# Performance work log

Hardware: AMD Instinct MI355X
Metric: run time of the kernel (lower is better)

## Reference

```python
import jax, jax.numpy as jnp
import numpy as np

D_IN = 1024
D_OUT = 1024
NUM_HEADS = 16
HEAD_DIM = D_OUT // NUM_HEADS


def setup_inputs() -> dict:
    key = jax.random.key(0)
    k1, k2, k3, k4 = jax.random.split(key, 4)
    x = jax.random.normal(k1, (2, 2048, D_IN), dtype=jnp.float32)
    # Linear weights stored torch-style [out_features, in_features]
    W_qkv = jax.random.normal(k2, (3 * D_OUT, D_IN), dtype=jnp.float32) * (1.0 / np.sqrt(D_IN))
    W_out = jax.random.normal(k3, (D_OUT, D_OUT), dtype=jnp.float32) * (1.0 / np.sqrt(D_OUT))
    b_out = jax.random.normal(k4, (D_OUT,), dtype=jnp.float32) * 0.01
    return {"x": x, "W_qkv": W_qkv, "W_out": W_out, "b_out": b_out}


def reference(x, W_qkv, W_out, b_out):
    b, s, _ = x.shape
    qkv = jnp.einsum('bsi,oi->bso', x, W_qkv)  # [b, s, 3*d_out]
    q, k, v = jnp.split(qkv, 3, axis=-1)
    def to_heads(t):
        return t.reshape(b, s, NUM_HEADS, HEAD_DIM).transpose(0, 2, 1, 3)
    q, k, v = to_heads(q), to_heads(k), to_heads(v)
    # NOTE: original module does NOT scale by 1/sqrt(head_dim)
    scores = jnp.einsum('bhqd,bhkd->bhqk', q, k)
    causal = jnp.tril(jnp.ones((s, s), dtype=bool))  # True = keep
    scores = jnp.where(causal[None, None], scores, -jnp.inf)
    attn = jax.nn.softmax(scores, axis=-1)
    ctx = jnp.einsum('bhqk,bhkd->bhqd', attn, v)
    ctx = ctx.transpose(0, 2, 1, 3).reshape(b, s, D_OUT)
    return jnp.einsum('bso,po->bsp', ctx, W_out) + b_out
```

## Files before the change

### kernel.cpp

```cpp
#include <hip/hip_runtime.h>
#include <cstdint>
#include <cstddef>


typedef __attribute__((ext_vector_type(8))) short bf16x8;
typedef __attribute__((ext_vector_type(4))) short bf16x4;
typedef __attribute__((ext_vector_type(4))) float f32x4;

#define LOG2E 1.44269504f

#define MFMA16(a, b, c) __builtin_amdgcn_mfma_f32_16x16x32_bf16((a), (b), (c), 0, 0, 0)

#if defined(__HIP_DEVICE_COMPILE__)
  #if __has_builtin(__builtin_amdgcn_mfma_f32_16x16x16bf16_1k)
    #define MFMAK16(a, b, c) __builtin_amdgcn_mfma_f32_16x16x16bf16_1k((a), (b), (c), 0, 0, 0)
  #elif __has_builtin(__builtin_amdgcn_mfma_f32_16x16x16_bf16)
    #define MFMAK16(a, b, c) __builtin_amdgcn_mfma_f32_16x16x16_bf16((a), (b), (c), 0, 0, 0)
  #else
    #error "no 16x16x16 bf16 MFMA builtin on device"
  #endif
#else
  #define MFMAK16(a, b, c) (c)
#endif

#define GLDS16(g, s)                                                        \
  __builtin_amdgcn_global_load_lds(                                         \
      (const __attribute__((address_space(1))) void*)(g),                   \
      (__attribute__((address_space(3))) void*)(s), 16, 0, 0)

#define ASYNC_BAR(N) asm volatile("s_waitcnt vmcnt(" #N ")\n\ts_barrier" ::: "memory")
#define BAR() asm volatile("s_barrier" ::: "memory")

static __device__ __forceinline__ float exp2_hw(float x) {
  float r;
  asm("v_exp_f32 %0, %1" : "=v"(r) : "v"(x));
  return r;
}
#define EXP2F(x) exp2_hw(x)

static __device__ __forceinline__ unsigned short f2bf(float f) {
  unsigned int u = __builtin_bit_cast(unsigned int, f);
  u += 0x7FFFu + ((u >> 16) & 1u);
  return (unsigned short)(u >> 16);
}

static __device__ __forceinline__ unsigned int pk2bf(float a, float b) {
  const unsigned int ua = __builtin_bit_cast(unsigned int, a) + 0x8000u;
  const unsigned int ub = __builtin_bit_cast(unsigned int, b) + 0x8000u;
  return __builtin_amdgcn_perm(ub, ua, 0x07060302);
}

__global__ __launch_bounds__(256) void cast_bf16(const float* __restrict__ x,
                                                 const float* __restrict__ wq,
                                                 const float* __restrict__ wo,
                                                 unsigned short* __restrict__ xb,
                                                 unsigned short* __restrict__ wqb,
                                                 unsigned short* __restrict__ wob)
{
  const int id = blockIdx.x * 256 + threadIdx.x;
  const float* src;
  unsigned short* dst;
  int off;
  if (id < 1048576)               { src = x;  dst = xb;  off = id; }
  else if (id < 1048576 + 786432) { src = wq; dst = wqb; off = id - 1048576; }
  else                            { src = wo; dst = wob; off = id - (1048576 + 786432); }
  float4 v = ((const float4*)src)[off];
  ushort4 o;
  o.x = f2bf(v.x); o.y = f2bf(v.y); o.z = f2bf(v.z); o.w = f2bf(v.w);
  ((ushort4*)dst)[off] = o;
}

#define MMAC(AF, BF, MS, NS)                                                       \
  do {                                                                             \
    __builtin_amdgcn_s_setprio(1);                                                 \
    if (swapped) {                                                                 \
      _Pragma("unroll")                                                            \
      for (int mt = 0; mt < 4; ++mt)                                               \
        _Pragma("unroll")                                                          \
        for (int nt = 0; nt < 2; ++nt) {                                           \
          acc[(MS)*4+mt][(NS)*2+nt] = MFMA16(BF[nt][0], AF[mt][0], acc[(MS)*4+mt][(NS)*2+nt]); \
          acc[(MS)*4+mt][(NS)*2+nt] = MFMA16(BF[nt][1], AF[mt][1], acc[(MS)*4+mt][(NS)*2+nt]); \
        }                                                                          \
    } else {                                                                       \
      _Pragma("unroll")                                                            \
      for (int mt = 0; mt < 4; ++mt)                                               \
        _Pragma("unroll")                                                          \
        for (int nt = 0; nt < 2; ++nt) {                                           \
          acc[(MS)*4+mt][(NS)*2+nt] = MFMA16(AF[mt][0], BF[nt][0], acc[(MS)*4+mt][(NS)*2+nt]); \
          acc[(MS)*4+mt][(NS)*2+nt] = MFMA16(AF[mt][1], BF[nt][1], acc[(MS)*4+mt][(NS)*2+nt]); \
        }                                                                          \
    }                                                                              \
    __builtin_amdgcn_s_setprio(0);                                                 \
  } while (0)

__global__ __launch_bounds__(512, 2) void gemm_qkv(const unsigned short* __restrict__ A,
                                                   const unsigned short* __restrict__ B,
                                                   unsigned short* __restrict__ Qb,
                                                   unsigned short* __restrict__ Kb,
                                                   unsigned short* __restrict__ Vt)
{
  __shared__ unsigned short pool[65536];

  const int tid  = threadIdx.x;
  const int wave = tid >> 6, lane = tid & 63, quad = lane >> 4, cl = lane & 15;
  const int wm = wave >> 2, wn = wave & 3;

  const int bid = blockIdx.x;
  const int xcd = bid & 7, j = bid >> 3;
  const int mb = (xcd >> 1) * 4 + j / 6;
  const int nb = (xcd & 1) * 6 + j % 6;
  const int m0 = mb * 256, n0 = nb * 256;
  const int part = nb >> 2;
  const bool swapped = (part < 2);

  const int lrow = lane >> 3;
  const int sg   = (lane & 7) ^ lrow;

  auto stageA = [&](int h0, int buf, int k0) {
    #pragma unroll
    for (int ii = 0; ii < 2; ++ii) {
      const int r0 = h0 + wave * 16 + ii * 8;
      GLDS16(A + (size_t)(m0 + r0 + lrow) * 1024 + k0 + sg * 8,
             &pool[buf * 32768 + r0 * 64]);
    }
  };
  auto stageB = [&](int h0, int buf, int k0) {
    #pragma unroll
    for (int ii = 0; ii < 2; ++ii) {
      const int r0 = h0 + wave * 16 + ii * 8;
      GLDS16(B + (size_t)(n0 + r0 + lrow) * 1024 + k0 + sg * 8,
             &pool[buf * 32768 + 16384 + r0 * 64]);
    }
  };

  const int rswz = cl & 7;
  auto loadA = [&](bf16x8 (&af)[4][2], int msub, int b) {
    const unsigned short* base = &pool[b * 32768];
    #pragma unroll
    for (int mt = 0; mt < 4; ++mt) {
      const int row = wm * 128 + msub * 64 + mt * 16 + cl;
      #pragma unroll
      for (int kk = 0; kk < 2; ++kk)
        af[mt][kk] = *(const bf16x8*)&base[row * 64 + ((kk * 4 + quad) ^ rswz) * 8];
    }
  };
  auto loadB = [&](bf16x8 (&bf)[2][2], int nsub, int b) {
    const unsigned short* base = &pool[b * 32768 + 16384];
    #pragma unroll
    for (int nt = 0; nt < 2; ++nt) {
      const int row = wn * 64 + nsub * 32 + nt * 16 + cl;
      #pragma unroll
      for (int kk = 0; kk < 2; ++kk)
        bf[nt][kk] = *(const bf16x8*)&base[row * 64 + ((kk * 4 + quad) ^ rswz) * 8];
    }
  };

  f32x4 acc[8][4];
  #pragma unroll
  for (int i = 0; i < 8; ++i)
    #pragma unroll
    for (int jj = 0; jj < 4; ++jj)
      #pragma unroll
      for (int r = 0; r < 4; ++r) acc[i][jj][r] = 0.f;

  stageB(0,   0, 0);
  stageA(0,   0, 0);
  stageB(128, 0, 0);
  stageA(128, 0, 0);
  stageB(0,   1, 64);
  stageA(0,   1, 64);

  #pragma unroll 1
  for (int t = 0; t < 16; ++t) {
    const int b = t & 1, bn = b ^ 1;
    const int kc  = (t + 1) * 64;
    const int kc2 = (t + 2) * 64;

    bf16x8 af[4][2], bfA[2][2], bfB[2][2];

    if (t < 15) { ASYNC_BAR(4); } else { ASYNC_BAR(0); }
    loadA(af, 0, b);
    loadB(bfA, 0, b);
    if (t < 15) stageB(128, bn, kc);
    MMAC(af, bfA, 0, 0);

    loadB(bfB, 1, b);
    if (t < 15) stageA(128, bn, kc);
    MMAC(af, bfB, 0, 1);

    BAR();
    loadA(af, 1, b);
    if (t < 14) stageB(0, b, kc2);
    MMAC(af, bfB, 1, 1);

    BAR();
    if (t < 14) stageA(0, b, kc2);
    MMAC(af, bfA, 1, 0);
  }

  const int bb = m0 >> 11, ss = m0 & 2047;
  if (part < 2) {
    unsigned short* dst = (part == 0) ? Qb : Kb;
    const float sc2 = (part == 0) ? LOG2E : 1.0f;
    const int npb = (n0 & 1023) + wn * 64;
    #pragma unroll
    for (int mt = 0; mt < 8; ++mt) {
      const int m = ss + wm * 128 + mt * 16 + cl;
      #pragma unroll
      for (int nt = 0; nt < 4; ++nt) {
        const int np = npb + nt * 16 + quad * 4;
        const int hh = np >> 6, d0 = np & 63;
        ushort4 pk;
        pk.x = f2bf(acc[mt][nt][0] * sc2);
        pk.y = f2bf(acc[mt][nt][1] * sc2);
        pk.z = f2bf(acc[mt][nt][2] * sc2);
        pk.w = f2bf(acc[mt][nt][3] * sc2);
        *(ushort4*)&dst[((size_t)(bb * 16 + hh) * 2048 + m) * 64 + d0] = pk;
      }
    }
  } else {
    unsigned short* trans = pool;
    #pragma unroll 1
    for (int r = 0; r < 2; ++r) {
      __syncthreads();
      if ((wn >> 1) == r) {
        #pragma unroll
        for (int mt = 0; mt < 8; ++mt) {
          const int s_l = wm * 128 + mt * 16 + quad * 4;
          #pragma unroll
          for (int nt = 0; nt < 4; ++nt) {
            const int n_l = (wn & 1) * 64 + nt * 16 + cl;
            ushort4 pk;
            pk.x = f2bf(acc[mt][nt][0]); pk.y = f2bf(acc[mt][nt][1]);
            pk.z = f2bf(acc[mt][nt][2]); pk.w = f2bf(acc[mt][nt][3]);
            *(ushort4*)&trans[n_l * 264 + s_l] = pk;
          }
        }
      }
      __syncthreads();
      const int row = tid >> 2, q4 = tid & 3;
      const int nv = (n0 & 1023) + r * 128 + row;
      const int hh = nv >> 6, d = nv & 63;
      unsigned short* drow = Vt + ((size_t)(bb * 16 + hh) * 64 + d) * 2048 + ss + q4 * 64;
      #pragma unroll
      for (int i = 0; i < 8; ++i)
        *(bf16x8*)(drow + i * 8) = *(const bf16x8*)&trans[row * 264 + q4 * 64 + i * 8];
    }
  }
}

__global__ __launch_bounds__(256) void gemm_obt(const unsigned short* __restrict__ A,
                                                const unsigned short* __restrict__ B,
                                                const float* __restrict__ bias,
                                                float* __restrict__ OutF)
{
  __shared__ unsigned short pool[24576];

  const int tid  = threadIdx.x;
  const int wave = tid >> 6, lane = tid & 63, quad = lane >> 4, cl = lane & 15;
  const int wm = wave >> 1, wn = wave & 1;
  const int m0 = blockIdx.y * 128, n0 = blockIdx.x * 128;
  const int sr = lane >> 2, sc = lane & 3;

  f32x4 acc[4][4];
  #pragma unroll
  for (int i = 0; i < 4; ++i)
    #pragma unroll
    for (int j = 0; j < 4; ++j)
      #pragma unroll
      for (int r = 0; r < 4; ++r) acc[i][j][r] = 0.f;

  const int scs = (sc ^ ((sr >> 1) & 3)) * 8;
  const int rchunk = (quad ^ ((cl >> 1) & 3)) * 8;

  auto stage = [&](int k0, int buf) {
    unsigned short* As = pool + buf * 8192;
    unsigned short* Bs = As + 4096;
    #pragma unroll
    for (int ii = 0; ii < 2; ++ii) {
      const int r = wave * 32 + ii * 16 + sr;
      GLDS16(A + (size_t)(m0 + r) * 1024 + k0 + scs, &As[(wave * 32 + ii * 16) * 32]);
      GLDS16(B + (size_t)(n0 + r) * 1024 + k0 + scs, &Bs[(wave * 32 + ii * 16) * 32]);
    }
  };

  stage(0, 0);
  stage(32, 1);
  int cur = 0;
  #pragma unroll 1
  for (int it = 0; it < 32; ++it) {
    if (it + 2 < 32) {
      ASYNC_BAR(4);
      const int bnx = (cur == 0) ? 2 : cur - 1;
      stage((it + 2) * 32, bnx);
    } else if (it + 1 < 32) {
      ASYNC_BAR(4);
    } else {
      ASYNC_BAR(0);
    }

    const unsigned short* As = pool + cur * 8192;
    const unsigned short* Bs = As + 4096;
    bf16x8 af[4], bfr[4];
    #pragma unroll
    for (int mt = 0; mt < 4; ++mt)
      af[mt] = *(const bf16x8*)&As[(wm * 64 + mt * 16 + cl) * 32 + rchunk];
    #pragma unroll
    for (int nt = 0; nt < 4; ++nt)
      bfr[nt] = *(const bf16x8*)&Bs[(wn * 64 + nt * 16 + cl) * 32 + rchunk];

    __builtin_amdgcn_s_setprio(1);
    #pragma unroll
    for (int mt = 0; mt < 4; ++mt)
      #pragma unroll
      for (int nt = 0; nt < 4; ++nt)
        acc[mt][nt] = MFMA16(bfr[nt], af[mt], acc[mt][nt]);
    __builtin_amdgcn_s_setprio(0);
    cur = (cur == 2) ? 0 : cur + 1;
  }

  #pragma unroll
  for (int mt = 0; mt < 4; ++mt) {
    const int m = m0 + wm * 64 + mt * 16 + cl;
    #pragma unroll
    for (int nt = 0; nt < 4; ++nt) {
      const int n = n0 + wn * 64 + nt * 16 + quad * 4;
      const float4 bv = *(const float4*)(bias + n);
      float4 o;
      o.x = acc[mt][nt][0] + bv.x; o.y = acc[mt][nt][1] + bv.y;
      o.z = acc[mt][nt][2] + bv.z; o.w = acc[mt][nt][3] + bv.w;
      *(float4*)&OutF[(size_t)m * 1024 + n] = o;
    }
  }
}

__global__ __launch_bounds__(512) void attn_mfma(const unsigned short* __restrict__ Qb,
                                                 const unsigned short* __restrict__ Kb,
                                                 const unsigned short* __restrict__ Vt,
                                                 unsigned short* __restrict__ CTX)
{
  __shared__ unsigned short Ksm[2][2][64 * 64];
  __shared__ unsigned short Vsm[2][2][64 * 64];

  const int tid  = threadIdx.x;
  const int wave = tid >> 6, lane = tid & 63, quad = lane >> 4, cl = lane & 15;
  const int g = wave & 3, sp = wave >> 2;

  const int L  = blockIdx.x;
  const int bh = 4 * (L & 7) + ((L >> 3) & 3);
  const int b  = bh >> 4, h = bh & 15;
  const int pp = 31 - (L >> 5);
  const int G  = pp * 4 + g;
  const int qb = G * 16;
  const size_t base = (size_t)bh * (2048 * 64);

  bf16x8 qf[2];
  #pragma unroll
  for (int dk = 0; dk < 2; ++dk)
    qf[dk] = *(const bf16x8*)(Qb + base + (size_t)(qb + cl) * 64 + dk * 32 + quad * 8);

  f32x4 oacc[4];
  #pragma unroll
  for (int dt = 0; dt < 4; ++dt)
    #pragma unroll
    for (int r = 0; r < 4; ++r) oacc[dt][r] = 0.f;
  float lr[4] = {};

  bf16x4 ones4;
  #pragma unroll
  for (int k = 0; k < 4; ++k) ones4[k] = (short)0x3F80;

  const int lrow  = lane >> 3;
  const int lslot = (lane & 7) ^ lrow;
  const int nch = pp + 1;
  const int nrd = (nch + 1) >> 1;

  auto stageKV = [&](int ch, int buf, int sub) {
    const int j64 = ch * 64;
    const int r0 = wave * 8;
    GLDS16(Kb + base + (size_t)(j64 + r0 + lrow) * 64 + lslot * 8,
           &Ksm[buf][sub][r0 * 64]);
    GLDS16(Vt + base + (size_t)(r0 + lrow) * 2048 + j64 + lslot * 8,
           &Vsm[buf][sub][r0 * 64]);
  };

  stageKV(0, 0, 0);
  stageKV(1, 0, 1);

  #pragma unroll 1
  for (int t = 0; t < nrd; ++t) {
    ASYNC_BAR(0);
    if (t + 1 < nrd) {
      stageKV(2 * t + 2, (t + 1) & 1, 0);
      stageKV(2 * t + 3, (t + 1) & 1, 1);
    }

    {
      const int ch = 2 * t + sp;
      const unsigned short* Kc = Ksm[t & 1][sp];
      const unsigned short* Vc = Vsm[t & 1][sp];
      const int j64c = ch * 64;

      #pragma unroll
      for (int jli = 0; jli < 2; ++jli) {
        const int jg0 = j64c + jli * 32;
        if (jg0 > qb + 15) continue;
        const int jl = jli * 32;

        bf16x8 kf[2][2];
        #pragma unroll
        for (int jf = 0; jf < 2; ++jf)
          #pragma unroll
          for (int dk = 0; dk < 2; ++dk) {
            const int jrow = jl + jf * 16 + cl;
            const int slot = (dk * 4 + quad) ^ (cl & 7);
            kf[jf][dk] = *(const bf16x8*)&Kc[jrow * 64 + slot * 8];
          }

        f32x4 st[2];
        __builtin_amdgcn_s_setprio(1);
        #pragma unroll
        for (int jf = 0; jf < 2; ++jf) {
          f32x4 z;
          #pragma unroll
          for (int r = 0; r < 4; ++r) z[r] = 0.f;
          z = MFMA16(kf[jf][0], qf[0], z);
          st[jf] = MFMA16(kf[jf][1], qf[1], z);
        }
        __builtin_amdgcn_s_setprio(0);

        const bool diag = (jg0 + 32 > qb);
        uint2 w[2];
        #pragma unroll
        for (int jf = 0; jf < 2; ++jf) {
          float pv[4];
          if (diag) {
            const int qg = qb + cl;
            #pragma unroll
            for (int r = 0; r < 4; ++r) {
              const int jg = jg0 + jf * 16 + quad * 4 + r;
              pv[r] = (jg <= qg) ? EXP2F(st[jf][r]) : 0.f;
            }
          } else {
            #pragma unroll
            for (int r = 0; r < 4; ++r) pv[r] = EXP2F(st[jf][r]);
          }
          w[jf].x = pk2bf(pv[0], pv[1]);
          w[jf].y = pk2bf(pv[2], pv[3]);
        }
        const bf16x4 pf0 = __builtin_bit_cast(bf16x4, w[0]);
        const bf16x4 pf1 = __builtin_bit_cast(bf16x4, w[1]);

        bf16x4 vf[2][4];
        #pragma unroll
        for (int jf = 0; jf < 2; ++jf) {
          const int slog = (jl >> 3) + jf * 2 + (quad >> 1);
          const int soff = ((slog ^ (cl & 7)) << 3) + ((quad & 1) << 2);
          #pragma unroll
          for (int dt = 0; dt < 4; ++dt) {
            const int d = dt * 16 + cl;
            vf[jf][dt] = *(const bf16x4*)&Vc[d * 64 + soff];
          }
        }

        __builtin_amdgcn_s_setprio(1);
        {
          f32x4 ls;
          #pragma unroll
          for (int r = 0; r < 4; ++r) ls[r] = 0.f;
          ls = MFMAK16(pf0, ones4, ls);
          ls = MFMAK16(pf1, ones4, ls);
          #pragma unroll
          for (int r = 0; r < 4; ++r) lr[r] += ls[r];
          #pragma unroll
          for (int dt = 0; dt < 4; ++dt) {
            oacc[dt] = MFMAK16(pf0, vf[0][dt], oacc[dt]);
            oacc[dt] = MFMAK16(pf1, vf[1][dt], oacc[dt]);
          }
        }
        __builtin_amdgcn_s_setprio(0);
      }
    }
  }

  __syncthreads();
  float* scr = reinterpret_cast<float*>(&Ksm[0][0][0]);
  const int si = (g * 64 + lane) * 20;
  if (sp == 1) {
    #pragma unroll
    for (int dt = 0; dt < 4; ++dt)
      *(f32x4*)&scr[si + dt * 4] = oacc[dt];
    #pragma unroll
    for (int r = 0; r < 4; ++r) scr[si + 16 + r] = lr[r];
  }
  __syncthreads();
  if (sp == 0) {
    #pragma unroll
    for (int dt = 0; dt < 4; ++dt) {
      const f32x4 o2 = *(const f32x4*)&scr[si + dt * 4];
      #pragma unroll
      for (int r = 0; r < 4; ++r) oacc[dt][r] += o2[r];
    }
    float inv[4];
    #pragma unroll
    for (int r = 0; r < 4; ++r) inv[r] = 1.f / (lr[r] + scr[si + 16 + r]);
    #pragma unroll
    for (int dt = 0; dt < 4; ++dt)
      #pragma unroll
      for (int r = 0; r < 4; ++r)
        CTX[(size_t)(b * 2048 + qb + quad * 4 + r) * 1024 +
            h * 64 + dt * 16 + cl] = f2bf(oacc[dt][r] * inv[r]);
  }
}

extern "C" void kernel_launch(void* const* d_in, const int* in_sizes, int n_in,
                              void* d_out, int out_size, void* d_ws, size_t ws_size,
                              hipStream_t stream)
{
  const float* x    = (const float*)d_in[0];
  const float* Wqkv = (const float*)d_in[1];
  const float* Wout = (const float*)d_in[2];
  const float* bout = (const float*)d_in[3];
  float* out = (float*)d_out;

  char* ws = (char*)d_ws;
  unsigned short* xb  = (unsigned short*)(ws);
  unsigned short* wqb = (unsigned short*)(ws + 8388608);
  unsigned short* wob = (unsigned short*)(ws + 14680064);
  unsigned short* Qb  = (unsigned short*)(ws + 16777216);
  unsigned short* Kb  = (unsigned short*)(ws + 25165824);
  unsigned short* Vt  = (unsigned short*)(ws + 33554432);
  unsigned short* CTX = (unsigned short*)(ws + 41943040);

  cast_bf16<<<dim3(8192), dim3(256), 0, stream>>>(x, Wqkv, Wout, xb, wqb, wob);

  gemm_qkv<<<dim3(192), dim3(512), 0, stream>>>(xb, wqb, Qb, Kb, Vt);

  attn_mfma<<<dim3(1024), dim3(512), 0, stream>>>(Qb, Kb, Vt, CTX);

  gemm_obt<<<dim3(8, 32), dim3(256), 0, stream>>>(CTX, wob, bout, out);
}
```

Measured before the change: 175.0 us.

## Split attention key range across four wave groups with 1024-thread blocks

The attention kernel now launches 1024 threads per block, so four wave groups (sp=0..3) each process a different 64-key chunk per round instead of two. K and V staging is divided between waves 0-7 (K) and waves 8-15 (V), and shared memory is doubled to hold four chunks per buffer. The final reduction sums partial outputs and row sums from three groups. This shortens the per-block serial key loop, at the cost of more LDS per block, lower block occupancy per CU, and a larger cross-wave reduction.

New measurement: 183.2 us. +4.7%, slower.

```diff
diff --git a/kernel.cpp b/kernel.cpp
--- a/kernel.cpp
+++ b/kernel.cpp
@@ -334,13 +334,13 @@
   }
 }
 
-__global__ __launch_bounds__(512) void attn_mfma(const unsigned short* __restrict__ Qb,
-                                                 const unsigned short* __restrict__ Kb,
-                                                 const unsigned short* __restrict__ Vt,
-                                                 unsigned short* __restrict__ CTX)
+__global__ __launch_bounds__(1024) void attn_mfma(const unsigned short* __restrict__ Qb,
+                                                  const unsigned short* __restrict__ Kb,
+                                                  const unsigned short* __restrict__ Vt,
+                                                  unsigned short* __restrict__ CTX)
 {
-  __shared__ unsigned short Ksm[2][2][64 * 64];
-  __shared__ unsigned short Vsm[2][2][64 * 64];
+  __shared__ unsigned short Ksm[2][4][64 * 64];
+  __shared__ unsigned short Vsm[2][4][64 * 64];
 
   const int tid  = threadIdx.x;
   const int wave = tid >> 6, lane = tid & 63, quad = lane >> 4, cl = lane & 15;
@@ -373,30 +373,36 @@
   const int lrow  = lane >> 3;
   const int lslot = (lane & 7) ^ lrow;
   const int nch = pp + 1;
-  const int nrd = (nch + 1) >> 1;
-
-  auto stageKV = [&](int ch, int buf, int sub) {
-    const int j64 = ch * 64;
-    const int r0 = wave * 8;
-    GLDS16(Kb + base + (size_t)(j64 + r0 + lrow) * 64 + lslot * 8,
-           &Ksm[buf][sub][r0 * 64]);
-    GLDS16(Vt + base + (size_t)(r0 + lrow) * 2048 + j64 + lslot * 8,
-           &Vsm[buf][sub][r0 * 64]);
+  const int nrd = (nch + 3) >> 2;
+
+  auto stageRound = [&](int t, int buf) {
+    const int r0 = (wave & 7) * 8;
+    if (wave < 8) {
+      #pragma unroll
+      for (int s = 0; s < 4; ++s) {
+        const int j64 = (4 * t + s) * 64;
+        GLDS16(Kb + base + (size_t)(j64 + r0 + lrow) * 64 + lslot * 8,
+               &Ksm[buf][s][r0 * 64]);
+      }
+    } else {
+      #pragma unroll
+      for (int s = 0; s < 4; ++s) {
+        const int j64 = (4 * t + s) * 64;
+        GLDS16(Vt + base + (size_t)(r0 + lrow) * 2048 + j64 + lslot * 8,
+               &Vsm[buf][s][r0 * 64]);
+      }
+    }
   };
 
-  stageKV(0, 0, 0);
-  stageKV(1, 0, 1);
+  stageRound(0, 0);
 
   #pragma unroll 1
   for (int t = 0; t < nrd; ++t) {
     ASYNC_BAR(0);
-    if (t + 1 < nrd) {
-      stageKV(2 * t + 2, (t + 1) & 1, 0);
-      stageKV(2 * t + 3, (t + 1) & 1, 1);
-    }
+    if (t + 1 < nrd) stageRound(t + 1, (t + 1) & 1);
 
     {
-      const int ch = 2 * t + sp;
+      const int ch = 4 * t + sp;
       const unsigned short* Kc = Ksm[t & 1][sp];
       const unsigned short* Vc = Vsm[t & 1][sp];
       const int j64c = ch * 64;
@@ -485,8 +491,8 @@
 
   __syncthreads();
   float* scr = reinterpret_cast<float*>(&Ksm[0][0][0]);
-  const int si = (g * 64 + lane) * 20;
-  if (sp == 1) {
+  if (sp > 0) {
+    const int si = (((sp - 1) * 4 + g) * 64 + lane) * 20;
     #pragma unroll
     for (int dt = 0; dt < 4; ++dt)
       *(f32x4*)&scr[si + dt * 4] = oacc[dt];
@@ -496,14 +502,20 @@
   __syncthreads();
   if (sp == 0) {
     #pragma unroll
-    for (int dt = 0; dt < 4; ++dt) {
-      const f32x4 o2 = *(const f32x4*)&scr[si + dt * 4];
-      #pragma unroll
-      for (int r = 0; r < 4; ++r) oacc[dt][r] += o2[r];
+    for (int k = 0; k < 3; ++k) {
+      const int si = ((k * 4 + g) * 64 + lane) * 20;
+      #pragma unroll
+      for (int dt = 0; dt < 4; ++dt) {
+        const f32x4 o2 = *(const f32x4*)&scr[si + dt * 4];
+        #pragma unroll
+        for (int r = 0; r < 4; ++r) oacc[dt][r] += o2[r];
+      }
+      #pragma unroll
+      for (int r = 0; r < 4; ++r) lr[r] += scr[si + 16 + r];
     }
     float inv[4];
     #pragma unroll
-    for (int r = 0; r < 4; ++r) inv[r] = 1.f / (lr[r] + scr[si + 16 + r]);
+    for (int r = 0; r < 4; ++r) inv[r] = 1.f / lr[r];
     #pragma unroll
     for (int dt = 0; dt < 4; ++dt)
       #pragma unroll
@@ -536,7 +548,7 @@
 
   gemm_qkv<<<dim3(192), dim3(512), 0, stream>>>(xb, wqb, Qb, Kb, Vt);
 
-  attn_mfma<<<dim3(1024), dim3(512), 0, stream>>>(Qb, Kb, Vt, CTX);
+  attn_mfma<<<dim3(1024), dim3(1024), 0, stream>>>(Qb, Kb, Vt, CTX);
 
   gemm_obt<<<dim3(8, 32), dim3(256), 0, stream>>>(CTX, wob, bout, out);
 }
```

## Restructure output projection GEMM with 8 waves, BK=64 and interleaved half-tile staging

Applied to the files above, without the earlier changes.

Rewrites the output-projection GEMM to use 512 threads (2x4 wave grid) with a K-step of 64 and a new XOR swizzle. Global-to-LDS staging is split into half-tiles that are issued between MFMA groups, so the next stage's loads overlap compute within one iteration using a two-buffer scheme. This aims to hide load latency and raise occupancy on a small, short-K GEMM. In exchange it adds extra barriers per iteration, and the buffer-reuse ordering is delicate.

Measured after the change: 174.2 us. About the same (-0.4%).

```diff
diff --git a/kernel.cpp b/kernel.cpp
--- a/kernel.cpp
+++ b/kernel.cpp
@@ -249,82 +249,110 @@
   }
 }
 
-__global__ __launch_bounds__(256) void gemm_obt(const unsigned short* __restrict__ A,
-                                                const unsigned short* __restrict__ B,
-                                                const float* __restrict__ bias,
-                                                float* __restrict__ OutF)
+__global__ __launch_bounds__(512, 4) void gemm_obt(const unsigned short* __restrict__ A,
+                                                   const unsigned short* __restrict__ B,
+                                                   const float* __restrict__ bias,
+                                                   float* __restrict__ OutF)
 {
-  __shared__ unsigned short pool[24576];
+  __shared__ unsigned short pool[32768];
 
   const int tid  = threadIdx.x;
   const int wave = tid >> 6, lane = tid & 63, quad = lane >> 4, cl = lane & 15;
-  const int wm = wave >> 1, wn = wave & 1;
+  const int wm = wave >> 2, wn = wave & 3;
   const int m0 = blockIdx.y * 128, n0 = blockIdx.x * 128;
-  const int sr = lane >> 2, sc = lane & 3;
-
-  f32x4 acc[4][4];
+
+  const int lrow = lane >> 3;
+  const int sg   = (lane & 7) ^ lrow;
+
+  auto stageA = [&](int h0, int buf, int k0) {
+    const int r0 = h0 + wave * 8;
+    GLDS16(A + (size_t)(m0 + r0 + lrow) * 1024 + k0 + sg * 8,
+           &pool[buf * 16384 + r0 * 64]);
+  };
+  auto stageB = [&](int h0, int buf, int k0) {
+    const int r0 = h0 + wave * 8;
+    GLDS16(B + (size_t)(n0 + r0 + lrow) * 1024 + k0 + sg * 8,
+           &pool[buf * 16384 + 8192 + r0 * 64]);
+  };
+
+  const int rswz = cl & 7;
+  auto loadA = [&](bf16x8 (&af)[2][2], int msub, int b) {
+    const unsigned short* base = &pool[b * 16384];
+    #pragma unroll
+    for (int mt = 0; mt < 2; ++mt) {
+      const int row = wm * 64 + msub * 32 + mt * 16 + cl;
+      #pragma unroll
+      for (int kk = 0; kk < 2; ++kk)
+        af[mt][kk] = *(const bf16x8*)&base[row * 64 + ((kk * 4 + quad) ^ rswz) * 8];
+    }
+  };
+  auto loadB = [&](bf16x8 (&bf)[2], int nsub, int b) {
+    const unsigned short* base = &pool[b * 16384 + 8192];
+    const int row = wn * 32 + nsub * 16 + cl;
+    #pragma unroll
+    for (int kk = 0; kk < 2; ++kk)
+      bf[kk] = *(const bf16x8*)&base[row * 64 + ((kk * 4 + quad) ^ rswz) * 8];
+  };
+
+  f32x4 acc[4][2];
   #pragma unroll
   for (int i = 0; i < 4; ++i)
     #pragma unroll
-    for (int j = 0; j < 4; ++j)
-      #pragma unroll
-      for (int r = 0; r < 4; ++r) acc[i][j][r] = 0.f;
-
-  const int scs = (sc ^ ((sr >> 1) & 3)) * 8;
-  const int rchunk = (quad ^ ((cl >> 1) & 3)) * 8;
-
-  auto stage = [&](int k0, int buf) {
-    unsigned short* As = pool + buf * 8192;
-    unsigned short* Bs = As + 4096;
-    #pragma unroll
-    for (int ii = 0; ii < 2; ++ii) {
-      const int r = wave * 32 + ii * 16 + sr;
-      GLDS16(A + (size_t)(m0 + r) * 1024 + k0 + scs, &As[(wave * 32 + ii * 16) * 32]);
-      GLDS16(B + (size_t)(n0 + r) * 1024 + k0 + scs, &Bs[(wave * 32 + ii * 16) * 32]);
-    }
-  };
-
-  stage(0, 0);
-  stage(32, 1);
-  int cur = 0;
+    for (int jj = 0; jj < 2; ++jj)
+      #pragma unroll
+      for (int r = 0; r < 4; ++r) acc[i][jj][r] = 0.f;
+
+  auto OMMA = [&](const bf16x8 (&af)[2][2], const bf16x8 (&bf)[2], int ms, int ns) {
+    __builtin_amdgcn_s_setprio(1);
+    #pragma unroll
+    for (int mt = 0; mt < 2; ++mt) {
+      acc[ms * 2 + mt][ns] = MFMA16(bf[0], af[mt][0], acc[ms * 2 + mt][ns]);
+      acc[ms * 2 + mt][ns] = MFMA16(bf[1], af[mt][1], acc[ms * 2 + mt][ns]);
+    }
+    __builtin_amdgcn_s_setprio(0);
+  };
+
+  stageB(0,  0, 0);
+  stageA(0,  0, 0);
+  stageB(64, 0, 0);
+  stageA(64, 0, 0);
+  stageB(0,  1, 64);
+  stageA(0,  1, 64);
+
   #pragma unroll 1
-  for (int it = 0; it < 32; ++it) {
-    if (it + 2 < 32) {
-      ASYNC_BAR(4);
-      const int bnx = (cur == 0) ? 2 : cur - 1;
-      stage((it + 2) * 32, bnx);
-    } else if (it + 1 < 32) {
-      ASYNC_BAR(4);
-    } else {
-      ASYNC_BAR(0);
-    }
-
-    const unsigned short* As = pool + cur * 8192;
-    const unsigned short* Bs = As + 4096;
-    bf16x8 af[4], bfr[4];
-    #pragma unroll
-    for (int mt = 0; mt < 4; ++mt)
-      af[mt] = *(const bf16x8*)&As[(wm * 64 + mt * 16 + cl) * 32 + rchunk];
-    #pragma unroll
-    for (int nt = 0; nt < 4; ++nt)
-      bfr[nt] = *(const bf16x8*)&Bs[(wn * 64 + nt * 16 + cl) * 32 + rchunk];
-
-    __builtin_amdgcn_s_setprio(1);
-    #pragma unroll
-    for (int mt = 0; mt < 4; ++mt)
-      #pragma unroll
-      for (int nt = 0; nt < 4; ++nt)
-        acc[mt][nt] = MFMA16(bfr[nt], af[mt], acc[mt][nt]);
-    __builtin_amdgcn_s_setprio(0);
-    cur = (cur == 2) ? 0 : cur + 1;
+  for (int t = 0; t < 16; ++t) {
+    const int b = t & 1, bn = b ^ 1;
+    const int kc  = (t + 1) * 64;
+    const int kc2 = (t + 2) * 64;
+
+    bf16x8 af[2][2], bfA[2], bfB[2];
+
+    if (t < 15) { ASYNC_BAR(2); } else { ASYNC_BAR(0); }
+    loadA(af, 0, b);
+    loadB(bfA, 0, b);
+    if (t < 15) stageB(64, bn, kc);
+    OMMA(af, bfA, 0, 0);
+
+    loadB(bfB, 1, b);
+    if (t < 15) stageA(64, bn, kc);
+    OMMA(af, bfB, 0, 1);
+
+    BAR();
+    loadA(af, 1, b);
+    if (t < 14) stageB(0, b, kc2);
+    OMMA(af, bfB, 1, 1);
+
+    BAR();
+    if (t < 14) stageA(0, b, kc2);
+    OMMA(af, bfA, 1, 0);
   }
 
   #pragma unroll
   for (int mt = 0; mt < 4; ++mt) {
     const int m = m0 + wm * 64 + mt * 16 + cl;
     #pragma unroll
-    for (int nt = 0; nt < 4; ++nt) {
-      const int n = n0 + wn * 64 + nt * 16 + quad * 4;
+    for (int nt = 0; nt < 2; ++nt) {
+      const int n = n0 + wn * 32 + nt * 16 + quad * 4;
       const float4 bv = *(const float4*)(bias + n);
       float4 o;
       o.x = acc[mt][nt][0] + bv.x; o.y = acc[mt][nt][1] + bv.y;
@@ -538,5 +566,5 @@
 
   attn_mfma<<<dim3(1024), dim3(512), 0, stream>>>(Qb, Kb, Vt, CTX);
 
-  gemm_obt<<<dim3(8, 32), dim3(256), 0, stream>>>(CTX, wob, bout, out);
-}
+  gemm_obt<<<dim3(8, 32), dim3(512), 0, stream>>>(CTX, wob, bout, out);
+}
```
